# Performance work log

Hardware: AMD Instinct MI355X
Metric: run time of the kernel (lower is better)

Reference implementation:

```python
import jax, jax.numpy as jnp
import numpy as np

N_QUBITS = 4
N_LAYERS = 2
DIM = 2 ** N_QUBITS  # 16
BATCH, INPUT_SIZE, HIDDEN_SIZE = 65536, 128, 512

# PennyLane default.qubit convention: wire 0 is the most significant bit.
def _cnot_perm(c, t, n=N_QUBITS):
    idx = np.arange(2 ** n)
    cbit = (idx >> (n - 1 - c)) & 1
    return np.where(cbit == 1, idx ^ (1 << (n - 1 - t)), idx)

# ring of CNOTs: control j -> target (j+1)%n
CNOT_PERMS = [jnp.asarray(_cnot_perm(j, (j + 1) % N_QUBITS)) for j in range(N_QUBITS)]
_idx = np.arange(DIM)
Z_SIGNS = jnp.asarray(np.stack([1.0 - 2.0 * ((_idx >> (N_QUBITS - 1 - j)) & 1) for j in range(N_QUBITS)], axis=1).astype(np.float32))  # [16, 4]


def _rx(t):
    c = jnp.cos(t / 2).astype(jnp.complex64)
    s = (-1j * jnp.sin(t / 2)).astype(jnp.complex64)
    return jnp.stack([jnp.stack([c, s]), jnp.stack([s, c])])


def _ry(t):
    c = jnp.cos(t / 2).astype(jnp.complex64)
    s = jnp.sin(t / 2).astype(jnp.complex64)
    return jnp.stack([jnp.stack([c, -s]), jnp.stack([s, c])])


def _rz(t):
    e = jnp.exp(-0.5j * t.astype(jnp.complex64))
    z = jnp.zeros((), jnp.complex64)
    return jnp.stack([jnp.stack([e, z]), jnp.stack([z, jnp.conj(e)])])


def _apply_1q(state, gate, j, n=N_QUBITS):
    # state: [B, 2^n] complex; gate: [2,2] (shared) or [B,2,2] (per-sample)
    B = state.shape[0]
    st = state.reshape(B, 2 ** j, 2, 2 ** (n - 1 - j))
    if gate.ndim == 2:
        st = jnp.einsum('ij,bajc->baic', gate, st)
    else:
        st = jnp.einsum('bij,bajc->baic', gate, st)
    return st.reshape(B, 2 ** n)


def _qlayer(angles, qweights):
    # Batched 4-qubit state-vector sim of the PennyLane circuit.
    # angles: [B, 4] float32 (RY embedding); qweights: [2, 4, 3]
    B = angles.shape[0]
    state = jnp.zeros((B, DIM), jnp.complex64).at[:, 0].set(1.0)
    c = jnp.cos(angles / 2).astype(jnp.complex64)
    s = jnp.sin(angles / 2).astype(jnp.complex64)
    for j in range(N_QUBITS):
        gate = jnp.stack([jnp.stack([c[:, j], -s[:, j]], -1), jnp.stack([s[:, j], c[:, j]], -1)], -2)  # [B,2,2]
        state = _apply_1q(state, gate, j)
    for l in range(N_LAYERS):
        for j in range(N_QUBITS):
            state = state[:, CNOT_PERMS[j]]
        for j in range(N_QUBITS):
            state = _apply_1q(state, _rx(qweights[l, j, 0]), j)
            state = _apply_1q(state, _ry(qweights[l, j, 1]), j)
            state = _apply_1q(state, _rz(qweights[l, j, 2]), j)
    probs = state.real ** 2 + state.imag ** 2  # [B, 16]
    return probs @ Z_SIGNS  # [B, 4] expval(PauliZ_j)


def _gate(combined, pw, pb, qw, lw, lb):
    ang = combined @ pw.T + pb  # [B, 4]
    # torch original runs the circuit on detached numpy and wraps the result in
    # torch.tensor -> no gradient flows through the quantum layer.
    q = jax.lax.stop_gradient(_qlayer(ang, qw))
    return q @ lw.T + lb  # [B, hidden]


GATES = ('forget', 'input', 'output', 'cell')


def setup_inputs() -> dict:
    key = jax.random.key(0)
    ks = jax.random.split(key, 3 + 3 * len(GATES))
    inp = {
        'x': jax.random.normal(ks[0], (BATCH, INPUT_SIZE), jnp.float32),
        'h_prev': jax.random.normal(ks[1], (BATCH, HIDDEN_SIZE), jnp.float32),
        'c_prev': jax.random.normal(ks[2], (BATCH, HIDDEN_SIZE), jnp.float32),
    }
    for i, g in enumerate(GATES):
        k0, k1, k2 = ks[3 + 3 * i], ks[4 + 3 * i], ks[5 + 3 * i]
        inp[g + '_proj_w'] = jax.random.normal(k0, (N_QUBITS, INPUT_SIZE + HIDDEN_SIZE), jnp.float32) * 0.02
        inp[g + '_proj_b'] = jnp.zeros((N_QUBITS,), jnp.float32)
        inp[g + '_qw'] = jax.random.normal(k1, (N_LAYERS, N_QUBITS, 3), jnp.float32) * 0.1
        inp[g + '_lin_w'] = jax.random.normal(k2, (HIDDEN_SIZE, N_QUBITS), jnp.float32) * 0.1
        inp[g + '_lin_b'] = jnp.zeros((HIDDEN_SIZE,), jnp.float32)
    return inp


def reference(x, h_prev, c_prev,
              forget_proj_w, forget_proj_b, forget_qw, forget_lin_w, forget_lin_b,
              input_proj_w, input_proj_b, input_qw, input_lin_w, input_lin_b,
              output_proj_w, output_proj_b, output_qw, output_lin_w, output_lin_b,
              cell_proj_w, cell_proj_b, cell_qw, cell_lin_w, cell_lin_b):
    combined = jnp.concatenate([x, h_prev], axis=1)  # [B, in+hid]
    f = jax.nn.sigmoid(_gate(combined, forget_proj_w, forget_proj_b, forget_qw, forget_lin_w, forget_lin_b))
    i = jax.nn.sigmoid(_gate(combined, input_proj_w, input_proj_b, input_qw, input_lin_w, input_lin_b))
    o = jax.nn.sigmoid(_gate(combined, output_proj_w, output_proj_b, output_qw, output_lin_w, output_lin_b))
    g = jnp.tanh(_gate(combined, cell_proj_w, cell_proj_b, cell_qw, cell_lin_w, cell_lin_b))
    c_next = f * c_prev + i * g
    h_next = o * jnp.tanh(c_next)
    return (h_next, c_next)
```

## Files before the change

kernel.cpp:

```cpp
#include <hip/hip_runtime.h>
#include <math.h>

#define BATCHN 65536
#define INPUTN 128
#define HIDDENN 512
#define CATN 640
#define ROWS_LSTM 32

typedef float f2v __attribute__((ext_vector_type(2)));

__global__ void k_build_u(const float* __restrict__ qwF, const float* __restrict__ qwI,
                          const float* __restrict__ qwO, const float* __restrict__ qwC,
                          float2* __restrict__ U) {
  int t = threadIdx.x;
  if (t >= 64) return;
  int g = t >> 4, col = t & 15;
  const float* qw = (g == 0) ? qwF : (g == 1) ? qwI : (g == 2) ? qwO : qwC;

  float sr[16], si[16];
#pragma unroll
  for (int i = 0; i < 16; i++) { sr[i] = (i == col) ? 1.f : 0.f; si[i] = 0.f; }

#pragma unroll
  for (int l = 0; l < 2; l++) {
#pragma unroll
    for (int j = 0; j < 4; j++) {
      const int bc = 8 >> j;
      const int bt = 8 >> ((j + 1) & 3);
      float tr[16], ti[16];
#pragma unroll
      for (int i = 0; i < 16; i++) {
        int src = (i & bc) ? (i ^ bt) : i;
        tr[i] = sr[src]; ti[i] = si[src];
      }
#pragma unroll
      for (int i = 0; i < 16; i++) { sr[i] = tr[i]; si[i] = ti[i]; }
    }
#pragma unroll
    for (int j = 0; j < 4; j++) {
      const int bit = 8 >> j;
      const float thx = qw[(l * 4 + j) * 3 + 0] * 0.5f;
      const float thy = qw[(l * 4 + j) * 3 + 1] * 0.5f;
      const float thz = qw[(l * 4 + j) * 3 + 2] * 0.5f;
      float c, s;
      c = cosf(thx); s = sinf(thx);
#pragma unroll
      for (int i = 0; i < 16; i++) if (!(i & bit)) {
        const int k2 = i | bit;
        const float ar = sr[i], ai = si[i], br = sr[k2], bi = si[k2];
        sr[i]  = c * ar + s * bi;  si[i]  = c * ai - s * br;
        sr[k2] = c * br + s * ai;  si[k2] = c * bi - s * ar;
      }
      c = cosf(thy); s = sinf(thy);
#pragma unroll
      for (int i = 0; i < 16; i++) if (!(i & bit)) {
        const int k2 = i | bit;
        const float ar = sr[i], ai = si[i], br = sr[k2], bi = si[k2];
        sr[i]  = c * ar - s * br;  si[i]  = c * ai - s * bi;
        sr[k2] = s * ar + c * br;  si[k2] = s * ai + c * bi;
      }
      c = cosf(thz); s = sinf(thz);
#pragma unroll
      for (int i = 0; i < 16; i++) if (!(i & bit)) {
        const int k2 = i | bit;
        const float ar = sr[i], ai = si[i], br = sr[k2], bi = si[k2];
        sr[i]  = c * ar + s * ai;  si[i]  = c * ai - s * ar;
        sr[k2] = c * br - s * bi;  si[k2] = c * bi + s * br;
      }
    }
  }
#pragma unroll
  for (int m = 0; m < 16; m++)
    U[(g * 16 + m) * 16 + col] = make_float2(sr[m], si[m]);
}

__global__ __launch_bounds__(256) void k_proj_q(
    const float* __restrict__ x, const float* __restrict__ hprev,
    const float* __restrict__ pwF, const float* __restrict__ pbF,
    const float* __restrict__ pwI, const float* __restrict__ pbI,
    const float* __restrict__ pwO, const float* __restrict__ pbO,
    const float* __restrict__ pwC, const float* __restrict__ pbC,
    const float2* __restrict__ U, float* __restrict__ qv) {
  __shared__ float4 smem[2560];
  const int tid = threadIdx.x;
  const int w = tid >> 6;
  const int l = tid & 63;
  const size_t row = (size_t)blockIdx.x * 64 + l;

  const float* pwg = (w == 0) ? pwF : (w == 1) ? pwI : (w == 2) ? pwO : pwC;
#pragma unroll
  for (int i = 0; i < 10; ++i)
    smem[w * 640 + l + i * 64] = ((const float4*)pwg)[l + i * 64];
  __syncthreads();

  float acc[16];
#pragma unroll
  for (int j = 0; j < 16; j++) acc[j] = 0.f;

  auto kstep = [&](int ss, float4 a) {
#pragma unroll
    for (int g = 0; g < 4; ++g)
#pragma unroll
      for (int o = 0; o < 4; ++o) {
        const float4 wv = smem[g * 640 + o * 160 + w * 40 + ss];
        acc[g * 4 + o] += a.x * wv.x + a.y * wv.y + a.z * wv.z + a.w * wv.w;
      }
  };

  if (w == 0) {
    const float* xr = x + row * INPUTN;
#pragma unroll 8
    for (int ss = 0; ss < 32; ++ss) kstep(ss, *(const float4*)(xr + ss * 4));
    const float* hr = hprev + row * HIDDENN;
#pragma unroll
    for (int ss = 32; ss < 40; ++ss) kstep(ss, *(const float4*)(hr + (ss - 32) * 4));
  } else {
    const float* hr = hprev + row * HIDDENN + (w * 160 - INPUTN);
#pragma unroll 8
    for (int ss = 0; ss < 40; ++ss) kstep(ss, *(const float4*)(hr + ss * 4));
  }

  __syncthreads();
  float* part = (float*)smem;
#pragma unroll
  for (int j4 = 0; j4 < 4; ++j4)
    *(float4*)&part[(w * 64 + l) * 20 + j4 * 4] =
        make_float4(acc[j4 * 4], acc[j4 * 4 + 1], acc[j4 * 4 + 2], acc[j4 * 4 + 3]);
  __syncthreads();

  const float* pbg = (w == 0) ? pbF : (w == 1) ? pbI : (w == 2) ? pbO : pbC;
  float ang[4] = {pbg[0], pbg[1], pbg[2], pbg[3]};
#pragma unroll
  for (int s = 0; s < 4; ++s) {
    const float4 p = *(const float4*)&part[(s * 64 + l) * 20 + w * 4];
    ang[0] += p.x; ang[1] += p.y; ang[2] += p.z; ang[3] += p.w;
  }

  float cs[4], sn[4];
#pragma unroll
  for (int j = 0; j < 4; j++) __sincosf(ang[j] * 0.5f, &sn[j], &cs[j]);
  float psi[16];
#pragma unroll
  for (int c16 = 0; c16 < 16; c16++) {
    float p = ((c16 & 8) ? sn[0] : cs[0]);
    p *= ((c16 & 4) ? sn[1] : cs[1]);
    p *= ((c16 & 2) ? sn[2] : cs[2]);
    p *= ((c16 & 1) ? sn[3] : cs[3]);
    psi[c16] = p;
  }
  const float2* Ug = U + w * 256;
  float q0 = 0.f, q1 = 0.f, q2 = 0.f, q3 = 0.f;
#pragma unroll
  for (int m = 0; m < 16; m++) {
    float ssr = 0.f, ssi = 0.f;
#pragma unroll
    for (int c16 = 0; c16 < 16; c16++) {
      const float2 u = Ug[m * 16 + c16];
      ssr += u.x * psi[c16];
      ssi += u.y * psi[c16];
    }
    const float p = ssr * ssr + ssi * ssi;
    q0 = (m & 8) ? q0 - p : q0 + p;
    q1 = (m & 4) ? q1 - p : q1 + p;
    q2 = (m & 2) ? q2 - p : q2 + p;
    q3 = (m & 1) ? q3 - p : q3 + p;
  }
  *(float4*)(qv + row * 16 + w * 4) = make_float4(q0, q1, q2, q3);
}

__device__ __forceinline__ float sigmf(float v) {
  return __builtin_amdgcn_rcpf(1.f + __expf(-v));
}
__device__ __forceinline__ float tanhfast(float v) {
  return 1.f - 2.f * __builtin_amdgcn_rcpf(__expf(2.f * v) + 1.f);
}

__global__ __launch_bounds__(256) void k_lstm(
    const float* __restrict__ qv, const float* __restrict__ cprev,
    const float* __restrict__ lwF, const float* __restrict__ lbF,
    const float* __restrict__ lwI, const float* __restrict__ lbI,
    const float* __restrict__ lwO, const float* __restrict__ lbO,
    const float* __restrict__ lwC, const float* __restrict__ lbC,
    float* __restrict__ out) {
  const int tid = threadIdx.x;
  const int h0 = tid * 2;
  const int rb = blockIdx.x * ROWS_LSTM;

  float4 wF[2], wI[2], wO[2], wC[2];
  float bFv[2], bIv[2], bOv[2], bCv[2];
#pragma unroll
  for (int hh = 0; hh < 2; ++hh) {
    const int hp = h0 + hh;
    wF[hh] = *(const float4*)(lwF + (size_t)hp * 4);
    wI[hh] = *(const float4*)(lwI + (size_t)hp * 4);
    wO[hh] = *(const float4*)(lwO + (size_t)hp * 4);
    wC[hh] = *(const float4*)(lwC + (size_t)hp * 4);
    bFv[hh] = lbF[hp]; bIv[hh] = lbI[hp]; bOv[hh] = lbO[hp]; bCv[hh] = lbC[hp];
  }

#pragma unroll 2
  for (int it = 0; it < ROWS_LSTM; ++it) {
    const int r = rb + it;
    const float* q = qv + (size_t)r * 16;
    const float4 qF = *(const float4*)(q);
    const float4 qI = *(const float4*)(q + 4);
    const float4 qO = *(const float4*)(q + 8);
    const float4 qC = *(const float4*)(q + 12);

    const f2v cp = __builtin_nontemporal_load(
        (const f2v*)(cprev + (size_t)r * HIDDENN + h0));
    float hn[2], cn[2];
#pragma unroll
    for (int hh = 0; hh < 2; ++hh) {
      const float pf = bFv[hh] + wF[hh].x * qF.x + wF[hh].y * qF.y + wF[hh].z * qF.z + wF[hh].w * qF.w;
      const float pi = bIv[hh] + wI[hh].x * qI.x + wI[hh].y * qI.y + wI[hh].z * qI.z + wI[hh].w * qI.w;
      const float po = bOv[hh] + wO[hh].x * qO.x + wO[hh].y * qO.y + wO[hh].z * qO.z + wO[hh].w * qO.w;
      const float pg = bCv[hh] + wC[hh].x * qC.x + wC[hh].y * qC.y + wC[hh].z * qC.z + wC[hh].w * qC.w;
      const float f  = sigmf(pf);
      const float ii = sigmf(pi);
      const float oo = sigmf(po);
      const float gg = tanhfast(pg);
      const float cc = f * cp[hh] + ii * gg;
      cn[hh] = cc;
      hn[hh] = oo * tanhfast(cc);
    }
    f2v hv; hv[0] = hn[0]; hv[1] = hn[1];
    f2v cv; cv[0] = cn[0]; cv[1] = cn[1];
    __builtin_nontemporal_store(hv, (f2v*)(out + (size_t)r * HIDDENN + h0));
    __builtin_nontemporal_store(cv,
        (f2v*)(out + (size_t)BATCHN * HIDDENN + (size_t)r * HIDDENN + h0));
  }
}

extern "C" void kernel_launch(void* const* d_in, const int* in_sizes, int n_in,
                              void* d_out, int out_size, void* d_ws, size_t ws_size,
                              hipStream_t stream) {
  const float* x  = (const float*)d_in[0];
  const float* h  = (const float*)d_in[1];
  const float* c  = (const float*)d_in[2];
  const float* pwF = (const float*)d_in[3];
  const float* pbF = (const float*)d_in[4];
  const float* qwF = (const float*)d_in[5];
  const float* lwF = (const float*)d_in[6];
  const float* lbF = (const float*)d_in[7];
  const float* pwI = (const float*)d_in[8];
  const float* pbI = (const float*)d_in[9];
  const float* qwI = (const float*)d_in[10];
  const float* lwI = (const float*)d_in[11];
  const float* lbI = (const float*)d_in[12];
  const float* pwO = (const float*)d_in[13];
  const float* pbO = (const float*)d_in[14];
  const float* qwO = (const float*)d_in[15];
  const float* lwO = (const float*)d_in[16];
  const float* lbO = (const float*)d_in[17];
  const float* pwC = (const float*)d_in[18];
  const float* pbC = (const float*)d_in[19];
  const float* qwC = (const float*)d_in[20];
  const float* lwC = (const float*)d_in[21];
  const float* lbC = (const float*)d_in[22];

  float* ws = (float*)d_ws;
  float* qv = ws;
  float2* U = (float2*)(ws + (size_t)BATCHN * 16);

  k_build_u<<<dim3(1), dim3(64), 0, stream>>>(qwF, qwI, qwO, qwC, U);
  k_proj_q<<<dim3(BATCHN / 64), dim3(256), 0, stream>>>(x, h, pwF, pbF, pwI, pbI,
                                                        pwO, pbO, pwC, pbC, U, qv);
  k_lstm<<<dim3(BATCHN / ROWS_LSTM), dim3(256), 0, stream>>>(qv, c, lwF, lbF, lwI, lbI,
                                                             lwO, lbO, lwC, lbC,
                                                             (float*)d_out);
}
```

Baseline: 163.5 us.

## Restructure projection GEMV so each thread holds weights in registers

Rewrites the projection stage of k_proj_q so that each of 16 output groups keeps one projection row slice in registers. A 16-lane group walks 64 rows, loading contiguous float4 chunks of x/h_prev (coalesced across lanes) and reducing with xor shuffles. This removes the shared-memory weight staging and the cross-warp partial-sum reduction, and replaces per-thread strided row reads with coalesced ones. The cost is a serial 64-iteration loop per block with shuffle reductions per row, and each input row is now loaded by all 16 output groups, relying on cache for reuse.

New measurement: 188.7 us. 1.15x slower.

```diff
diff --git a/kernel.cpp b/kernel.cpp
--- a/kernel.cpp
+++ b/kernel.cpp
@@ -81,60 +81,53 @@
     const float* __restrict__ pwO, const float* __restrict__ pbO,
     const float* __restrict__ pwC, const float* __restrict__ pbC,
     const float2* __restrict__ U, float* __restrict__ qv) {
-  __shared__ float4 smem[2560];
+  __shared__ float angL[64 * 17];
   const int tid = threadIdx.x;
-  const int w = tid >> 6;
-  const int l = tid & 63;
-  const size_t row = (size_t)blockIdx.x * 64 + l;
-
-  const float* pwg = (w == 0) ? pwF : (w == 1) ? pwI : (w == 2) ? pwO : pwC;
-#pragma unroll
-  for (int i = 0; i < 10; ++i)
-    smem[w * 640 + l + i * 64] = ((const float4*)pwg)[l + i * 64];
+  const int og = tid >> 4;
+  const int cg = tid & 15;
+  const int g = tid >> 6;
+  const int orow = og & 3;
+  const size_t rb = (size_t)blockIdx.x * 64;
+
+  const float* pw = (g == 0) ? pwF : (g == 1) ? pwI : (g == 2) ? pwO : pwC;
+  const float* pb = (g == 0) ? pbF : (g == 1) ? pbI : (g == 2) ? pbO : pbC;
+
+  float4 wr[10];
+  const float4* pwrow = (const float4*)(pw + orow * CATN);
+#pragma unroll
+  for (int i = 0; i < 10; ++i) wr[i] = pwrow[cg + 16 * i];
+
+  const float4* xf = (const float4*)x;
+  const float4* hf = (const float4*)hprev;
+
+#pragma unroll 1
+  for (int r = 0; r < 64; ++r) {
+    const size_t R = rb + r;
+    float4 ch[10];
+    ch[0] = xf[R * 32 + cg];
+    ch[1] = xf[R * 32 + cg + 16];
+#pragma unroll
+    for (int i = 2; i < 10; ++i) ch[i] = hf[R * 128 + cg + 16 * (i - 2)];
+
+    float a0 = 0.f, a1 = 0.f, a2 = 0.f, a3 = 0.f;
+#pragma unroll
+    for (int i = 0; i < 10; ++i) {
+      a0 += ch[i].x * wr[i].x;
+      a1 += ch[i].y * wr[i].y;
+      a2 += ch[i].z * wr[i].z;
+      a3 += ch[i].w * wr[i].w;
+    }
+    float acc = (a0 + a1) + (a2 + a3);
+#pragma unroll
+    for (int m = 1; m < 16; m <<= 1) acc += __shfl_xor(acc, m, 64);
+    if (cg == 0) angL[r * 17 + og] = acc;
+  }
   __syncthreads();
 
-  float acc[16];
-#pragma unroll
-  for (int j = 0; j < 16; j++) acc[j] = 0.f;
-
-  auto kstep = [&](int ss, float4 a) {
-#pragma unroll
-    for (int g = 0; g < 4; ++g)
-#pragma unroll
-      for (int o = 0; o < 4; ++o) {
-        const float4 wv = smem[g * 640 + o * 160 + w * 40 + ss];
-        acc[g * 4 + o] += a.x * wv.x + a.y * wv.y + a.z * wv.z + a.w * wv.w;
-      }
-  };
-
-  if (w == 0) {
-    const float* xr = x + row * INPUTN;
-#pragma unroll 8
-    for (int ss = 0; ss < 32; ++ss) kstep(ss, *(const float4*)(xr + ss * 4));
-    const float* hr = hprev + row * HIDDENN;
-#pragma unroll
-    for (int ss = 32; ss < 40; ++ss) kstep(ss, *(const float4*)(hr + (ss - 32) * 4));
-  } else {
-    const float* hr = hprev + row * HIDDENN + (w * 160 - INPUTN);
-#pragma unroll 8
-    for (int ss = 0; ss < 40; ++ss) kstep(ss, *(const float4*)(hr + ss * 4));
-  }
-
-  __syncthreads();
-  float* part = (float*)smem;
-#pragma unroll
-  for (int j4 = 0; j4 < 4; ++j4)
-    *(float4*)&part[(w * 64 + l) * 20 + j4 * 4] =
-        make_float4(acc[j4 * 4], acc[j4 * 4 + 1], acc[j4 * 4 + 2], acc[j4 * 4 + 3]);
-  __syncthreads();
-
-  const float* pbg = (w == 0) ? pbF : (w == 1) ? pbI : (w == 2) ? pbO : pbC;
-  float ang[4] = {pbg[0], pbg[1], pbg[2], pbg[3]};
-#pragma unroll
-  for (int s = 0; s < 4; ++s) {
-    const float4 p = *(const float4*)&part[(s * 64 + l) * 20 + w * 4];
-    ang[0] += p.x; ang[1] += p.y; ang[2] += p.z; ang[3] += p.w;
-  }
+  const int row = tid & 63;
+  float ang[4];
+#pragma unroll
+  for (int j = 0; j < 4; ++j) ang[j] = angL[row * 17 + g * 4 + j] + pb[j];
 
   float cs[4], sn[4];
 #pragma unroll
@@ -148,7 +141,7 @@
     p *= ((c16 & 1) ? sn[3] : cs[3]);
     psi[c16] = p;
   }
-  const float2* Ug = U + w * 256;
+  const float2* Ug = U + g * 256;
   float q0 = 0.f, q1 = 0.f, q2 = 0.f, q3 = 0.f;
 #pragma unroll
   for (int m = 0; m < 16; m++) {
@@ -165,7 +158,7 @@
     q2 = (m & 2) ? q2 - p : q2 + p;
     q3 = (m & 1) ? q3 - p : q3 + p;
   }
-  *(float4*)(qv + row * 16 + w * 4) = make_float4(q0, q1, q2, q3);
+  *(float4*)(qv + (rb + row) * 16 + g * 4) = make_float4(q0, q1, q2, q3);
 }
 
 __device__ __forceinline__ float sigmf(float v) {
```
